# Optimization experiments

Measured on AMD Instinct MI355X. Metric: run time of the kernel, lower is better.

The kernel has to match this reference:

```python
import jax, jax.numpy as jnp
import numpy as np

N, E, F_IN, H, D = 50000, 800000, 128, 4, 32
NEG_SLOPE = 0.2

def setup_inputs() -> dict:
    key = jax.random.key(0)
    ks = jax.random.split(key, 8)
    x = jax.random.normal(ks[0], (N, F_IN), dtype=jnp.float32)
    src = jax.random.randint(ks[1], (E,), 0, N, dtype=jnp.int32)
    dst = jax.random.randint(ks[2], (E,), 0, N, dtype=jnp.int32)
    s = 1.0 / np.sqrt(F_IN)
    W_src = jax.random.uniform(ks[3], (F_IN, H * D), jnp.float32, -s, s)
    b_src = jnp.zeros((H * D,), jnp.float32)
    W_dst = jax.random.uniform(ks[4], (F_IN, H * D), jnp.float32, -s, s)
    b_dst = jnp.zeros((H * D,), jnp.float32)
    attn = jax.random.normal(ks[5], (H, D), dtype=jnp.float32) / np.sqrt(D)
    return {"x": x, "src": src, "dst": dst, "W_src": W_src, "b_src": b_src,
            "W_dst": W_dst, "b_dst": b_dst, "attn": attn}

def reference(x, src, dst, W_src, b_src, W_dst, b_dst, attn):
    n = x.shape[0]
    # dense projections: [N, H, D]
    fs = (x @ W_src + b_src).reshape(n, H, D)
    fd = (x @ W_dst + b_dst).reshape(n, H, D)
    # GATv2 edge score: a^T leaky_relu(W_l x_u + W_r x_v)
    e = jax.nn.leaky_relu(fs[src] + fd[dst], NEG_SLOPE)  # [E, H, D]
    score = jnp.einsum('ehd,hd->eh', e, attn)            # [E, H]
    # segment softmax over incoming edges of each dst node
    smax = jax.ops.segment_max(score, dst, num_segments=n)
    smax = jnp.where(jnp.isfinite(smax), smax, 0.0)
    ex = jnp.exp(score - smax[dst])
    denom = jax.ops.segment_sum(ex, dst, num_segments=n)
    alpha = ex / denom[dst]                              # [E, H]
    # scatter-weighted aggregation of src features
    h = jax.ops.segment_sum(alpha[:, :, None] * fs[src], dst, num_segments=n)
    h = jax.nn.relu(h)                                   # activation=relu
    return h.reshape(n, H * D)
```

## Files before the change

kernel.cpp:

```cpp
#include <hip/hip_runtime.h>
#include <hip/hip_fp16.h>

#define NN 50000
#define NE 800000
#define FIN 128
#define NH 4
#define HD 32
#define FOUT 128
#define NEG 0.2f
#define NB_W    ((256 * FIN + 255) / 256)
#define N_GEMM  782
#define NBKT    98
#define CHUNK   4096
#define NCHUNK  ((NE + CHUNK - 1) / CHUNK)
#define GB_GRID 980
#define BCAP    12288

typedef __attribute__((ext_vector_type(8))) short bf16x8;
typedef __attribute__((ext_vector_type(4))) float f32x4;

__device__ __forceinline__ uint f2bf_u(float f) {
    uint u = __float_as_uint(f);
    u += 0x7FFF + ((u >> 16) & 1);
    return u >> 16;
}
__device__ __forceinline__ ushort f2bf(float f) { return (ushort)f2bf_u(f); }
__device__ __forceinline__ uint f2h_u(float f) {
    return (uint)__builtin_bit_cast(ushort, __float2half(f));
}

template<int CTRL>
__device__ __forceinline__ float dpp_add(float x) {
    int y = __builtin_amdgcn_update_dpp(0, __float_as_int(x), CTRL, 0xF, 0xF, false);
    return x + __int_as_float(y);
}
#define DPP_QUAD_XOR1 0xB1
#define DPP_QUAD_XOR2 0x4E

__device__ __forceinline__ __half2 u2h(uint u) { return __builtin_bit_cast(__half2, u); }
__device__ __forceinline__ uint h2u(__half2 h) { return __builtin_bit_cast(uint, h); }

__device__ __forceinline__ __half2 hmax2(__half2 a, __half2 b) {
    uint r, ua = h2u(a), ub = h2u(b);
    asm("v_pk_max_f16 %0, %1, %2" : "=v"(r) : "v"(ua), "v"(ub));
    return u2h(r);
}

__global__ __launch_bounds__(256) void hist_wt_k(
    const int* __restrict__ dst, int* __restrict__ chunk_hist,
    const float* __restrict__ Wsrc, const float* __restrict__ Wdst,
    ushort* __restrict__ Wt,
    const float* __restrict__ attn, __half* __restrict__ attn_h)
{
    __shared__ int hist[NBKT];
    const int b = blockIdx.x;
    const int tid = threadIdx.x;
    if (b < NCHUNK) {
        const int e0 = b * CHUNK;
        for (int t = tid; t < NBKT; t += 256) hist[t] = 0;
        __syncthreads();
        #pragma unroll
        for (int k = 0; k < 16; ++k) {
            const int e = e0 + k * 256 + tid;
            if (e < NE) atomicAdd(&hist[dst[e] >> 9], 1);
        }
        __syncthreads();
        for (int t = tid; t < NBKT; t += 256)
            chunk_hist[b * NBKT + t] = hist[t];
    } else {
        if (b == NCHUNK && tid < FOUT) attn_h[tid] = __float2half(attn[tid]);
        int t = (b - NCHUNK) * 256 + tid;
        if (t >= 256 * FIN) return;
        int n = t >> 7, k = t & 127;
        float v = (n < 128) ? Wsrc[k * 128 + n] : Wdst[k * 128 + (n - 128)];
        Wt[t] = f2bf(v);
    }
}

__global__ __launch_bounds__(256) void gemm_scatter_k(
    const float* __restrict__ x, const ushort* __restrict__ Wt,
    const float* __restrict__ bsrc, const float* __restrict__ bdst,
    __half* __restrict__ fsfd,
    const int* __restrict__ dst, const int* __restrict__ src,
    const int* __restrict__ chunk_hist, int* __restrict__ bkbase,
    uint* __restrict__ ebuf)
{
    __shared__ ushort As[64 * 128];
    __shared__ ushort Bs[64 * 128];
    __shared__ int ps[256];
    __shared__ int gbase[NBKT];
    __shared__ int lcur[NBKT];
    __shared__ int delta[NBKT];
    const int b = blockIdx.x;
    const int tid = threadIdx.x;

    if (b % 5 == 0) {
        const int chunk = b / 5;
        uint* stage = (uint*)As;

        int total = 0, part = 0;
        if (tid < NBKT) {
            for (int c = 0; c < NCHUNK; ++c) {
                const int h = chunk_hist[c * NBKT + tid];
                total += h;
                part += (c < chunk) ? h : 0;
            }
        }
        ps[tid] = (tid < NBKT) ? total : 0;
        __syncthreads();
        for (int off = 1; off < 256; off <<= 1) {
            int add = (tid >= off) ? ps[tid - off] : 0;
            __syncthreads();
            ps[tid] += add;
            __syncthreads();
        }
        if (tid < NBKT) gbase[tid] = (ps[tid] - total) + part;
        if (chunk == 0) {
            if (tid < NBKT) bkbase[tid] = ps[tid] - total;
            if (tid == 0) bkbase[NBKT] = NE;
        }
        if (tid < NBKT) lcur[tid] = 0;
        __syncthreads();

        const int e0 = chunk * CHUNK;
        int d[16], s[16];
        #pragma unroll
        for (int k = 0; k < 16; ++k) {
            const int e = e0 + k * 256 + tid;
            if (e < NE) {
                d[k] = dst[e];
                s[k] = src[e];
                atomicAdd(&lcur[d[k] >> 9], 1);
            } else d[k] = -1;
        }
        __syncthreads();

        const int lv = (tid < NBKT) ? lcur[tid] : 0;
        ps[tid] = lv;
        __syncthreads();
        for (int off = 1; off < 256; off <<= 1) {
            int add = (tid >= off) ? ps[tid - off] : 0;
            __syncthreads();
            ps[tid] += add;
            __syncthreads();
        }
        if (tid < NBKT) {
            const int loff = ps[tid] - lv;
            lcur[tid] = loff;
            delta[tid] = gbase[tid] - loff;
        }
        __syncthreads();

        #pragma unroll
        for (int k = 0; k < 16; ++k) {
            if (d[k] >= 0) {
                const int p = atomicAdd(&lcur[d[k] >> 9], 1);
                stage[p] = ((uint)d[k] << 16) | (uint)s[k];
            }
        }
        __syncthreads();

        const int cnt = (NE - e0 < CHUNK) ? (NE - e0) : CHUNK;
        for (int i = tid; i < cnt; i += 256) {
            const uint e = stage[i];
            ebuf[delta[e >> 25] + i] = e;
        }
        return;
    }

    const int g = b - b / 5 - 1;
    if (g >= N_GEMM) return;
    const int bm = g * 64;

    for (int q = tid; q < 64 * 16; q += 256) {
        int r = q >> 4, c16 = q & 15;
        int row = bm + r;
        uint4 o = make_uint4(0u, 0u, 0u, 0u);
        if (row < NN) {
            const float4 a = *(const float4*)&x[(size_t)row * FIN + c16 * 8];
            const float4 c = *(const float4*)&x[(size_t)row * FIN + c16 * 8 + 4];
            o.x = f2bf_u(a.x) | (f2bf_u(a.y) << 16);
            o.y = f2bf_u(a.z) | (f2bf_u(a.w) << 16);
            o.z = f2bf_u(c.x) | (f2bf_u(c.y) << 16);
            o.w = f2bf_u(c.z) | (f2bf_u(c.w) << 16);
        }
        int off = r * 256 + ((c16 * 16) ^ ((r & 7) << 4));
        *(uint4*)((char*)As + off) = o;
    }

    const int wid = tid >> 6, lane = tid & 63;
    const int wr = (wid >> 1) * 32, wc = (wid & 1) * 32;
    const int lrow = lane & 15;
    const int lk = (lane >> 4) * 16;

    #pragma unroll
    for (int ct = 0; ct < 4; ++ct) {
        if (ct > 0) __syncthreads();
        for (int q = tid; q < 64 * 16; q += 256) {
            int r = q >> 4, c16 = q & 15;
            uint4 v = *(const uint4*)&Wt[(ct * 64 + r) * FIN + c16 * 8];
            int off = r * 256 + ((c16 * 16) ^ ((r & 7) << 4));
            *(uint4*)((char*)Bs + off) = v;
        }
        __syncthreads();

        f32x4 acc[2][2] = {};
        #pragma unroll
        for (int kk = 0; kk < 4; ++kk) {
            bf16x8 a[2], bb[2];
            #pragma unroll
            for (int m = 0; m < 2; ++m) {
                int r = wr + m * 16 + lrow;
                int off = r * 256 + ((kk * 64 + lk) ^ ((r & 7) << 4));
                a[m] = *(bf16x8*)((char*)As + off);
            }
            #pragma unroll
            for (int n = 0; n < 2; ++n) {
                int r = wc + n * 16 + lrow;
                int off = r * 256 + ((kk * 64 + lk) ^ ((r & 7) << 4));
                bb[n] = *(bf16x8*)((char*)Bs + off);
            }
            #pragma unroll
            for (int m = 0; m < 2; ++m)
                #pragma unroll
                for (int n = 0; n < 2; ++n)
                    acc[m][n] = __builtin_amdgcn_mfma_f32_16x16x32_bf16(bb[n], a[m], acc[m][n], 0, 0, 0);
        }

        #pragma unroll
        for (int m = 0; m < 2; ++m) {
            const int grow = bm + wr + m * 16 + (lane & 15);
            if (grow >= NN) continue;
            #pragma unroll
            for (int n = 0; n < 2; ++n) {
                const int gcolb = ct * 64 + wc + n * 16 + (lane >> 4) * 4;
                const float4 b4 = (gcolb < 128) ? *(const float4*)&bsrc[gcolb]
                                                : *(const float4*)&bdst[gcolb - 128];
                uint lo = f2h_u(acc[m][n][0] + b4.x) | (f2h_u(acc[m][n][1] + b4.y) << 16);
                uint hi = f2h_u(acc[m][n][2] + b4.z) | (f2h_u(acc[m][n][3] + b4.w) << 16);
                *(uint2*)&fsfd[(size_t)grow * 256 + gcolb] = make_uint2(lo, hi);
            }
        }
    }
}

__global__ __launch_bounds__(256) void binB_k(
    const uint* __restrict__ ebuf, const int* __restrict__ bkbase,
    int* __restrict__ rowptr, ushort* __restrict__ nbr)
{
    __shared__ int cnt_s[512];
    __shared__ int ps[256];
    __shared__ ushort buf[BCAP];
    const int b = blockIdx.x;
    const int tid = threadIdx.x;
    const int node0 = b << 9;
    const int nodes = (node0 + 512 < NN) ? 512 : (NN - node0);
    const int segbase = bkbase[b];
    const int segend  = bkbase[b + 1];
    const int seglen  = segend - segbase;

    cnt_s[tid] = 0;
    cnt_s[tid + 256] = 0;
    __syncthreads();
    for (int i = segbase + tid; i < segend; i += 256)
        atomicAdd(&cnt_s[(int)(ebuf[i] >> 16) - node0], 1);
    __syncthreads();

    const int c0 = cnt_s[2 * tid], c1 = cnt_s[2 * tid + 1];
    const int pair = c0 + c1;
    ps[tid] = pair;
    __syncthreads();
    for (int off = 1; off < 256; off <<= 1) {
        int add = (tid >= off) ? ps[tid - off] : 0;
        __syncthreads();
        ps[tid] += add;
        __syncthreads();
    }
    const int ex = ps[tid] - pair;
    __syncthreads();
    cnt_s[2 * tid] = ex;
    cnt_s[2 * tid + 1] = ex + c0;
    if (2 * tid < nodes)     rowptr[node0 + 2 * tid]     = segbase + ex;
    if (2 * tid + 1 < nodes) rowptr[node0 + 2 * tid + 1] = segbase + ex + c0;
    if (b == NBKT - 1 && tid == 0) rowptr[NN] = segend;
    __syncthreads();

    if (seglen <= BCAP) {
        for (int i = segbase + tid; i < segend; i += 256) {
            const uint e = ebuf[i];
            const int d = (int)(e >> 16) - node0;
            const int p = atomicAdd(&cnt_s[d], 1);
            buf[p] = (ushort)(e & 0xffffu);
        }
        __syncthreads();
        for (int i = tid; i < seglen; i += 256)
            nbr[segbase + i] = buf[i];
    } else {
        for (int i = segbase + tid; i < segend; i += 256) {
            const uint e = ebuf[i];
            const int d = (int)(e >> 16) - node0;
            const int p = atomicAdd(&cnt_s[d], 1);
            nbr[segbase + p] = (ushort)(e & 0xffffu);
        }
    }
}

__global__ __launch_bounds__(256) void gat_node_k(
    const __half* __restrict__ fsfd, const __half* __restrict__ attn_h,
    const int* __restrict__ rowptr, const ushort* __restrict__ nbr,
    float* __restrict__ out)
{
    const int node = blockIdx.x * 4 + (threadIdx.x >> 6);
    const int lane = threadIdx.x & 63;
    const int ql = lane & 15;
    const int q  = lane >> 4;

    const uint4 ufd = *(const uint4*)&fsfd[(size_t)node * 256 + 128 + 8 * ql];
    const __half2 fd0 = u2h(ufd.x), fd1 = u2h(ufd.y), fd2 = u2h(ufd.z), fd3 = u2h(ufd.w);
    const uint4 uav = *(const uint4*)&attn_h[8 * ql];
    const __half2 av0 = u2h(uav.x), av1 = u2h(uav.y), av2 = u2h(uav.z), av3 = u2h(uav.w);
    const __half2 k02 = __float2half2_rn(NEG);

    const int beg = rowptr[node];
    const int end = rowptr[node + 1];

    float den = 0.f;
    __half2 acc0 = u2h(0), acc1 = u2h(0), acc2 = u2h(0), acc3 = u2h(0);

    for (int i = beg; i < end; i += 16) {
        #pragma unroll
        for (int j = 0; j < 4; ++j) {
            const int idx = i + 4 * j + q;
            const bool valid = idx < end;
            const int s = nbr[valid ? idx : end - 1];
            const uint4 u = *(const uint4*)&fsfd[(size_t)s * 256 + 8 * ql];
            const __half2 f0 = u2h(u.x), f1 = u2h(u.y), f2 = u2h(u.z), f3 = u2h(u.w);
            __half2 v0 = __hadd2(f0, fd0), v1 = __hadd2(f1, fd1);
            __half2 v2 = __hadd2(f2, fd2), v3 = __hadd2(f3, fd3);
            v0 = hmax2(v0, __hmul2(v0, k02));
            v1 = hmax2(v1, __hmul2(v1, k02));
            v2 = hmax2(v2, __hmul2(v2, k02));
            v3 = hmax2(v3, __hmul2(v3, k02));
            __half2 sch = __hmul2(v0, av0);
            sch = __hfma2(v1, av1, sch);
            sch = __hfma2(v2, av2, sch);
            sch = __hfma2(v3, av3, sch);
            float sc = __low2float(sch) + __high2float(sch);
            sc = dpp_add<DPP_QUAD_XOR1>(sc);
            sc = dpp_add<DPP_QUAD_XOR2>(sc);
            float ex = __expf(sc);
            ex = valid ? ex : 0.f;
            den += ex;
            const __half2 exh = __float2half2_rn(ex);
            acc0 = __hfma2(exh, f0, acc0);
            acc1 = __hfma2(exh, f1, acc1);
            acc2 = __hfma2(exh, f2, acc2);
            acc3 = __hfma2(exh, f3, acc3);
        }
    }

    den += __shfl_xor(den, 16, 64);
    den += __shfl_xor(den, 32, 64);
    uint ua0 = h2u(acc0), ua1 = h2u(acc1), ua2 = h2u(acc2), ua3 = h2u(acc3);
    ua0 = h2u(__hadd2(u2h(ua0), u2h((uint)__shfl_xor((int)ua0, 16, 64))));
    ua1 = h2u(__hadd2(u2h(ua1), u2h((uint)__shfl_xor((int)ua1, 16, 64))));
    ua2 = h2u(__hadd2(u2h(ua2), u2h((uint)__shfl_xor((int)ua2, 16, 64))));
    ua3 = h2u(__hadd2(u2h(ua3), u2h((uint)__shfl_xor((int)ua3, 16, 64))));
    ua0 = h2u(__hadd2(u2h(ua0), u2h((uint)__shfl_xor((int)ua0, 32, 64))));
    ua1 = h2u(__hadd2(u2h(ua1), u2h((uint)__shfl_xor((int)ua1, 32, 64))));
    ua2 = h2u(__hadd2(u2h(ua2), u2h((uint)__shfl_xor((int)ua2, 32, 64))));
    ua3 = h2u(__hadd2(u2h(ua3), u2h((uint)__shfl_xor((int)ua3, 32, 64))));

    if (q == 0) {
        const float inv = (den > 0.f) ? 1.f / den : 0.f;
        float4 o0, o1;
        o0.x = fmaxf(__low2float(u2h(ua0))  * inv, 0.f);
        o0.y = fmaxf(__high2float(u2h(ua0)) * inv, 0.f);
        o0.z = fmaxf(__low2float(u2h(ua1))  * inv, 0.f);
        o0.w = fmaxf(__high2float(u2h(ua1)) * inv, 0.f);
        o1.x = fmaxf(__low2float(u2h(ua2))  * inv, 0.f);
        o1.y = fmaxf(__high2float(u2h(ua2)) * inv, 0.f);
        o1.z = fmaxf(__low2float(u2h(ua3))  * inv, 0.f);
        o1.w = fmaxf(__high2float(u2h(ua3)) * inv, 0.f);
        *(float4*)&out[(size_t)node * FOUT + 8 * ql] = o0;
        *(float4*)&out[(size_t)node * FOUT + 8 * ql + 4] = o1;
    }
}

extern "C" void kernel_launch(void* const* d_in, const int* in_sizes, int n_in,
                              void* d_out, int out_size, void* d_ws, size_t ws_size,
                              hipStream_t stream)
{
    const float* x    = (const float*)d_in[0];
    const int*   src  = (const int*)d_in[1];
    const int*   dst  = (const int*)d_in[2];
    const float* Wsrc = (const float*)d_in[3];
    const float* bsrc = (const float*)d_in[4];
    const float* Wdst = (const float*)d_in[5];
    const float* bdst = (const float*)d_in[6];
    const float* attn = (const float*)d_in[7];
    float* out = (float*)d_out;

    ushort* Wt      = (ushort*)d_ws;
    __half* fsfd    = (__half*)(Wt + 256 * FIN);
    int* chunk_hist = (int*)(fsfd + (size_t)NN * 256);
    int* bkbase     = chunk_hist + NCHUNK * NBKT;
    int* rowptr     = bkbase + NBKT + 1;
    uint* ebuf      = (uint*)(rowptr + NN + 1);
    ushort* nbr     = (ushort*)(ebuf + NE);
    __half* attn_h  = (__half*)(nbr + NE);

    hist_wt_k<<<NCHUNK + NB_W, 256, 0, stream>>>(dst, chunk_hist, Wsrc, Wdst, Wt, attn, attn_h);
    gemm_scatter_k<<<GB_GRID, 256, 0, stream>>>(x, Wt, bsrc, bdst, fsfd,
                                                dst, src, chunk_hist, bkbase, ebuf);
    binB_k<<<NBKT, 256, 0, stream>>>(ebuf, bkbase, rowptr, nbr);
    gat_node_k<<<(NN + 3) / 4, 256, 0, stream>>>(fsfd, attn_h, rowptr, nbr, out);
}
```

Measured before the change: 86.93 us.

## Split GEMM stripes across scatter and binning kernels to overlap work

The projection GEMM is split into two halves. The first half is interleaved with the edge-scatter blocks in one kernel, and the second half with the per-bucket CSR binning blocks in the next kernel. Before, the binning kernel ran only 98 blocks on its own. Co-scheduling it with GEMM stripes is meant to fill the idle compute units and hide the binning and scatter latency. The binning buffer now reuses the GEMM shared-memory pool, which raises LDS use per block and may lower occupancy.

After: 86.93 us. Within noise of the previous version (+0.0%).

```diff
diff --git a/kernel.cpp b/kernel.cpp
--- a/kernel.cpp
+++ b/kernel.cpp
@@ -13,7 +13,8 @@
 #define NBKT    98
 #define CHUNK   4096
 #define NCHUNK  ((NE + CHUNK - 1) / CHUNK)
-#define GB_GRID 980
+#define GS1_GRID 587
+#define GS2_GRID 489
 #define BCAP    12288
 
 typedef __attribute__((ext_vector_type(8))) short bf16x8;
@@ -46,132 +47,12 @@
     return u2h(r);
 }
 
-__global__ __launch_bounds__(256) void hist_wt_k(
-    const int* __restrict__ dst, int* __restrict__ chunk_hist,
-    const float* __restrict__ Wsrc, const float* __restrict__ Wdst,
-    ushort* __restrict__ Wt,
-    const float* __restrict__ attn, __half* __restrict__ attn_h)
-{
-    __shared__ int hist[NBKT];
-    const int b = blockIdx.x;
-    const int tid = threadIdx.x;
-    if (b < NCHUNK) {
-        const int e0 = b * CHUNK;
-        for (int t = tid; t < NBKT; t += 256) hist[t] = 0;
-        __syncthreads();
-        #pragma unroll
-        for (int k = 0; k < 16; ++k) {
-            const int e = e0 + k * 256 + tid;
-            if (e < NE) atomicAdd(&hist[dst[e] >> 9], 1);
-        }
-        __syncthreads();
-        for (int t = tid; t < NBKT; t += 256)
-            chunk_hist[b * NBKT + t] = hist[t];
-    } else {
-        if (b == NCHUNK && tid < FOUT) attn_h[tid] = __float2half(attn[tid]);
-        int t = (b - NCHUNK) * 256 + tid;
-        if (t >= 256 * FIN) return;
-        int n = t >> 7, k = t & 127;
-        float v = (n < 128) ? Wsrc[k * 128 + n] : Wdst[k * 128 + (n - 128)];
-        Wt[t] = f2bf(v);
-    }
-}
-
-__global__ __launch_bounds__(256) void gemm_scatter_k(
+__device__ __forceinline__ void gemm_stripe(
+    ushort* As, ushort* Bs, const int tid, const int bm,
     const float* __restrict__ x, const ushort* __restrict__ Wt,
     const float* __restrict__ bsrc, const float* __restrict__ bdst,
-    __half* __restrict__ fsfd,
-    const int* __restrict__ dst, const int* __restrict__ src,
-    const int* __restrict__ chunk_hist, int* __restrict__ bkbase,
-    uint* __restrict__ ebuf)
-{
-    __shared__ ushort As[64 * 128];
-    __shared__ ushort Bs[64 * 128];
-    __shared__ int ps[256];
-    __shared__ int gbase[NBKT];
-    __shared__ int lcur[NBKT];
-    __shared__ int delta[NBKT];
-    const int b = blockIdx.x;
-    const int tid = threadIdx.x;
-
-    if (b % 5 == 0) {
-        const int chunk = b / 5;
-        uint* stage = (uint*)As;
-
-        int total = 0, part = 0;
-        if (tid < NBKT) {
-            for (int c = 0; c < NCHUNK; ++c) {
-                const int h = chunk_hist[c * NBKT + tid];
-                total += h;
-                part += (c < chunk) ? h : 0;
-            }
-        }
-        ps[tid] = (tid < NBKT) ? total : 0;
-        __syncthreads();
-        for (int off = 1; off < 256; off <<= 1) {
-            int add = (tid >= off) ? ps[tid - off] : 0;
-            __syncthreads();
-            ps[tid] += add;
-            __syncthreads();
-        }
-        if (tid < NBKT) gbase[tid] = (ps[tid] - total) + part;
-        if (chunk == 0) {
-            if (tid < NBKT) bkbase[tid] = ps[tid] - total;
-            if (tid == 0) bkbase[NBKT] = NE;
-        }
-        if (tid < NBKT) lcur[tid] = 0;
-        __syncthreads();
-
-        const int e0 = chunk * CHUNK;
-        int d[16], s[16];
-        #pragma unroll
-        for (int k = 0; k < 16; ++k) {
-            const int e = e0 + k * 256 + tid;
-            if (e < NE) {
-                d[k] = dst[e];
-                s[k] = src[e];
-                atomicAdd(&lcur[d[k] >> 9], 1);
-            } else d[k] = -1;
-        }
-        __syncthreads();
-
-        const int lv = (tid < NBKT) ? lcur[tid] : 0;
-        ps[tid] = lv;
-        __syncthreads();
-        for (int off = 1; off < 256; off <<= 1) {
-            int add = (tid >= off) ? ps[tid - off] : 0;
-            __syncthreads();
-            ps[tid] += add;
-            __syncthreads();
-        }
-        if (tid < NBKT) {
-            const int loff = ps[tid] - lv;
-            lcur[tid] = loff;
-            delta[tid] = gbase[tid] - loff;
-        }
-        __syncthreads();
-
-        #pragma unroll
-        for (int k = 0; k < 16; ++k) {
-            if (d[k] >= 0) {
-                const int p = atomicAdd(&lcur[d[k] >> 9], 1);
-                stage[p] = ((uint)d[k] << 16) | (uint)s[k];
-            }
-        }
-        __syncthreads();
-
-        const int cnt = (NE - e0 < CHUNK) ? (NE - e0) : CHUNK;
-        for (int i = tid; i < cnt; i += 256) {
-            const uint e = stage[i];
-            ebuf[delta[e >> 25] + i] = e;
-        }
-        return;
-    }
-
-    const int g = b - b / 5 - 1;
-    if (g >= N_GEMM) return;
-    const int bm = g * 64;
-
+    __half* __restrict__ fsfd)
+{
     for (int q = tid; q < 64 * 16; q += 256) {
         int r = q >> 4, c16 = q & 15;
         int row = bm + r;
@@ -244,65 +125,202 @@
     }
 }
 
-__global__ __launch_bounds__(256) void binB_k(
+__global__ __launch_bounds__(256) void hist_wt_k(
+    const int* __restrict__ dst, int* __restrict__ chunk_hist,
+    const float* __restrict__ Wsrc, const float* __restrict__ Wdst,
+    ushort* __restrict__ Wt,
+    const float* __restrict__ attn, __half* __restrict__ attn_h)
+{
+    __shared__ int hist[NBKT];
+    const int b = blockIdx.x;
+    const int tid = threadIdx.x;
+    if (b < NCHUNK) {
+        const int e0 = b * CHUNK;
+        for (int t = tid; t < NBKT; t += 256) hist[t] = 0;
+        __syncthreads();
+        #pragma unroll
+        for (int k = 0; k < 16; ++k) {
+            const int e = e0 + k * 256 + tid;
+            if (e < NE) atomicAdd(&hist[dst[e] >> 9], 1);
+        }
+        __syncthreads();
+        for (int t = tid; t < NBKT; t += 256)
+            chunk_hist[b * NBKT + t] = hist[t];
+    } else {
+        if (b == NCHUNK && tid < FOUT) attn_h[tid] = __float2half(attn[tid]);
+        int t = (b - NCHUNK) * 256 + tid;
+        if (t >= 256 * FIN) return;
+        int n = t >> 7, k = t & 127;
+        float v = (n < 128) ? Wsrc[k * 128 + n] : Wdst[k * 128 + (n - 128)];
+        Wt[t] = f2bf(v);
+    }
+}
+
+__global__ __launch_bounds__(256) void gs1_k(
+    const float* __restrict__ x, const ushort* __restrict__ Wt,
+    const float* __restrict__ bsrc, const float* __restrict__ bdst,
+    __half* __restrict__ fsfd,
+    const int* __restrict__ dst, const int* __restrict__ src,
+    const int* __restrict__ chunk_hist, int* __restrict__ bkbase,
+    uint* __restrict__ ebuf)
+{
+    __shared__ ushort pool[64 * 128 * 2];
+    __shared__ int ps[256];
+    __shared__ int gbase[NBKT];
+    __shared__ int lcur[NBKT];
+    __shared__ int delta[NBKT];
+    const int b = blockIdx.x;
+    const int tid = threadIdx.x;
+
+    if (b % 3 == 0) {
+        const int chunk = b / 3;
+        uint* stage = (uint*)pool;
+
+        int total = 0, part = 0;
+        if (tid < NBKT) {
+            for (int c = 0; c < NCHUNK; ++c) {
+                const int h = chunk_hist[c * NBKT + tid];
+                total += h;
+                part += (c < chunk) ? h : 0;
+            }
+        }
+        ps[tid] = (tid < NBKT) ? total : 0;
+        __syncthreads();
+        for (int off = 1; off < 256; off <<= 1) {
+            int add = (tid >= off) ? ps[tid - off] : 0;
+            __syncthreads();
+            ps[tid] += add;
+            __syncthreads();
+        }
+        if (tid < NBKT) gbase[tid] = (ps[tid] - total) + part;
+        if (chunk == 0) {
+            if (tid < NBKT) bkbase[tid] = ps[tid] - total;
+            if (tid == 0) bkbase[NBKT] = NE;
+        }
+        if (tid < NBKT) lcur[tid] = 0;
+        __syncthreads();
+
+        const int e0 = chunk * CHUNK;
+        int d[16], s[16];
+        #pragma unroll
+        for (int k = 0; k < 16; ++k) {
+            const int e = e0 + k * 256 + tid;
+            if (e < NE) {
+                d[k] = dst[e];
+                s[k] = src[e];
+                atomicAdd(&lcur[d[k] >> 9], 1);
+            } else d[k] = -1;
+        }
+        __syncthreads();
+
+        const int lv = (tid < NBKT) ? lcur[tid] : 0;
+        ps[tid] = lv;
+        __syncthreads();
+        for (int off = 1; off < 256; off <<= 1) {
+            int add = (tid >= off) ? ps[tid - off] : 0;
+            __syncthreads();
+            ps[tid] += add;
+            __syncthreads();
+        }
+        if (tid < NBKT) {
+            const int loff = ps[tid] - lv;
+            lcur[tid] = loff;
+            delta[tid] = gbase[tid] - loff;
+        }
+        __syncthreads();
+
+        #pragma unroll
+        for (int k = 0; k < 16; ++k) {
+            if (d[k] >= 0) {
+                const int p = atomicAdd(&lcur[d[k] >> 9], 1);
+                stage[p] = ((uint)d[k] << 16) | (uint)s[k];
+            }
+        }
+        __syncthreads();
+
+        const int cnt = (NE - e0 < CHUNK) ? (NE - e0) : CHUNK;
+        for (int i = tid; i < cnt; i += 256) {
+            const uint e = stage[i];
+            ebuf[delta[e >> 25] + i] = e;
+        }
+        return;
+    }
+
+    const int g = b - b / 3 - 1;
+    gemm_stripe(pool, pool + 64 * 128, tid, g * 64, x, Wt, bsrc, bdst, fsfd);
+}
+
+__global__ __launch_bounds__(256) void gs2_k(
+    const float* __restrict__ x, const ushort* __restrict__ Wt,
+    const float* __restrict__ bsrc, const float* __restrict__ bdst,
+    __half* __restrict__ fsfd,
     const uint* __restrict__ ebuf, const int* __restrict__ bkbase,
     int* __restrict__ rowptr, ushort* __restrict__ nbr)
 {
+    __shared__ ushort pool[64 * 128 * 2];
     __shared__ int cnt_s[512];
     __shared__ int ps[256];
-    __shared__ ushort buf[BCAP];
     const int b = blockIdx.x;
     const int tid = threadIdx.x;
-    const int node0 = b << 9;
-    const int nodes = (node0 + 512 < NN) ? 512 : (NN - node0);
-    const int segbase = bkbase[b];
-    const int segend  = bkbase[b + 1];
-    const int seglen  = segend - segbase;
-
-    cnt_s[tid] = 0;
-    cnt_s[tid + 256] = 0;
-    __syncthreads();
-    for (int i = segbase + tid; i < segend; i += 256)
-        atomicAdd(&cnt_s[(int)(ebuf[i] >> 16) - node0], 1);
-    __syncthreads();
-
-    const int c0 = cnt_s[2 * tid], c1 = cnt_s[2 * tid + 1];
-    const int pair = c0 + c1;
-    ps[tid] = pair;
-    __syncthreads();
-    for (int off = 1; off < 256; off <<= 1) {
-        int add = (tid >= off) ? ps[tid - off] : 0;
-        __syncthreads();
-        ps[tid] += add;
-        __syncthreads();
-    }
-    const int ex = ps[tid] - pair;
-    __syncthreads();
-    cnt_s[2 * tid] = ex;
-    cnt_s[2 * tid + 1] = ex + c0;
-    if (2 * tid < nodes)     rowptr[node0 + 2 * tid]     = segbase + ex;
-    if (2 * tid + 1 < nodes) rowptr[node0 + 2 * tid + 1] = segbase + ex + c0;
-    if (b == NBKT - 1 && tid == 0) rowptr[NN] = segend;
-    __syncthreads();
-
-    if (seglen <= BCAP) {
-        for (int i = segbase + tid; i < segend; i += 256) {
-            const uint e = ebuf[i];
-            const int d = (int)(e >> 16) - node0;
-            const int p = atomicAdd(&cnt_s[d], 1);
-            buf[p] = (ushort)(e & 0xffffu);
-        }
-        __syncthreads();
-        for (int i = tid; i < seglen; i += 256)
-            nbr[segbase + i] = buf[i];
-    } else {
-        for (int i = segbase + tid; i < segend; i += 256) {
-            const uint e = ebuf[i];
-            const int d = (int)(e >> 16) - node0;
-            const int p = atomicAdd(&cnt_s[d], 1);
-            nbr[segbase + p] = (ushort)(e & 0xffffu);
-        }
-    }
+
+    if (b % 5 == 0) {
+        const int bb = b / 5;
+        ushort* buf = pool;
+        const int node0 = bb << 9;
+        const int nodes = (node0 + 512 < NN) ? 512 : (NN - node0);
+        const int segbase = bkbase[bb];
+        const int segend  = bkbase[bb + 1];
+        const int seglen  = segend - segbase;
+
+        cnt_s[tid] = 0;
+        cnt_s[tid + 256] = 0;
+        __syncthreads();
+        for (int i = segbase + tid; i < segend; i += 256)
+            atomicAdd(&cnt_s[(int)(ebuf[i] >> 16) - node0], 1);
+        __syncthreads();
+
+        const int c0 = cnt_s[2 * tid], c1 = cnt_s[2 * tid + 1];
+        const int pair = c0 + c1;
+        ps[tid] = pair;
+        __syncthreads();
+        for (int off = 1; off < 256; off <<= 1) {
+            int add = (tid >= off) ? ps[tid - off] : 0;
+            __syncthreads();
+            ps[tid] += add;
+            __syncthreads();
+        }
+        const int ex = ps[tid] - pair;
+        __syncthreads();
+        cnt_s[2 * tid] = ex;
+        cnt_s[2 * tid + 1] = ex + c0;
+        if (2 * tid < nodes)     rowptr[node0 + 2 * tid]     = segbase + ex;
+        if (2 * tid + 1 < nodes) rowptr[node0 + 2 * tid + 1] = segbase + ex + c0;
+        if (bb == NBKT - 1 && tid == 0) rowptr[NN] = segend;
+        __syncthreads();
+
+        if (seglen <= BCAP) {
+            for (int i = segbase + tid; i < segend; i += 256) {
+                const uint e = ebuf[i];
+                const int d = (int)(e >> 16) - node0;
+                const int p = atomicAdd(&cnt_s[d], 1);
+                buf[p] = (ushort)(e & 0xffffu);
+            }
+            __syncthreads();
+            for (int i = tid; i < seglen; i += 256)
+                nbr[segbase + i] = buf[i];
+        } else {
+            for (int i = segbase + tid; i < segend; i += 256) {
+                const uint e = ebuf[i];
+                const int d = (int)(e >> 16) - node0;
+                const int p = atomicAdd(&cnt_s[d], 1);
+                nbr[segbase + p] = (ushort)(e & 0xffffu);
+            }
+        }
+        return;
+    }
+
+    const int g = 391 + (b - b / 5 - 1);
+    gemm_stripe(pool, pool + 64 * 128, tid, g * 64, x, Wt, bsrc, bdst, fsfd);
 }
 
 __global__ __launch_bounds__(256) void gat_node_k(
@@ -411,8 +429,9 @@
     __half* attn_h  = (__half*)(nbr + NE);
 
     hist_wt_k<<<NCHUNK + NB_W, 256, 0, stream>>>(dst, chunk_hist, Wsrc, Wdst, Wt, attn, attn_h);
-    gemm_scatter_k<<<GB_GRID, 256, 0, stream>>>(x, Wt, bsrc, bdst, fsfd,
-                                                dst, src, chunk_hist, bkbase, ebuf);
-    binB_k<<<NBKT, 256, 0, stream>>>(ebuf, bkbase, rowptr, nbr);
+    gs1_k<<<GS1_GRID, 256, 0, stream>>>(x, Wt, bsrc, bdst, fsfd,
+                                        dst, src, chunk_hist, bkbase, ebuf);
+    gs2_k<<<GS2_GRID, 256, 0, stream>>>(x, Wt, bsrc, bdst, fsfd,
+                                        ebuf, bkbase, rowptr, nbr);
     gat_node_k<<<(NN + 3) / 4, 256, 0, stream>>>(fsfd, attn_h, rowptr, nbr, out);
 }
```

## Pre-swizzle weights and async-load B tiles directly to LDS in GEMM

Applied to the files above, without the earlier changes.

The weight transpose kernel now writes weights in the XOR-swizzled LDS layout, so the GEMM can copy each 64-column B tile straight into shared memory with global_load_lds, skipping the register round trip. The next B tile's load is issued before the epilogue stores of the current tile so the two overlap. A fragments are hoisted into registers once and reused across all four column tiles. This costs more registers and extra barriers, and relies on the swizzle layout matching the LDS read pattern exactly.

Result: no change. 87.33 us (+0.5%).

```diff
diff --git a/kernel.cpp b/kernel.cpp
--- a/kernel.cpp
+++ b/kernel.cpp
@@ -18,6 +18,8 @@
 
 typedef __attribute__((ext_vector_type(8))) short bf16x8;
 typedef __attribute__((ext_vector_type(4))) float f32x4;
+typedef __attribute__((address_space(1))) const uint GMem;
+typedef __attribute__((address_space(3))) uint LMem;
 
 __device__ __forceinline__ uint f2bf_u(float f) {
     uint u = __float_as_uint(f);
@@ -49,7 +51,7 @@
 __global__ __launch_bounds__(256) void hist_wt_k(
     const int* __restrict__ dst, int* __restrict__ chunk_hist,
     const float* __restrict__ Wsrc, const float* __restrict__ Wdst,
-    ushort* __restrict__ Wt,
+    ushort* __restrict__ WtSw,
     const float* __restrict__ attn, __half* __restrict__ attn_h)
 {
     __shared__ int hist[NBKT];
@@ -73,12 +75,13 @@
         if (t >= 256 * FIN) return;
         int n = t >> 7, k = t & 127;
         float v = (n < 128) ? Wsrc[k * 128 + n] : Wdst[k * 128 + (n - 128)];
-        Wt[t] = f2bf(v);
+        const int idx = n * 128 + ((((k >> 3) ^ (n & 7))) << 3) + (k & 7);
+        WtSw[idx] = f2bf(v);
     }
 }
 
 __global__ __launch_bounds__(256) void gemm_scatter_k(
-    const float* __restrict__ x, const ushort* __restrict__ Wt,
+    const float* __restrict__ x, const ushort* __restrict__ WtSw,
     const float* __restrict__ bsrc, const float* __restrict__ bdst,
     __half* __restrict__ fsfd,
     const int* __restrict__ dst, const int* __restrict__ src,
@@ -193,27 +196,35 @@
     const int lrow = lane & 15;
     const int lk = (lane >> 4) * 16;
 
+    {
+        const char* gsrc = (const char*)WtSw;
+        #pragma unroll
+        for (int i = 0; i < 4; ++i) {
+            const int seg = i * 4 + wid;
+            __builtin_amdgcn_global_load_lds(
+                (GMem*)(gsrc + seg * 1024 + lane * 16),
+                (LMem*)((char*)Bs + seg * 1024),
+                16, 0, 0);
+        }
+    }
+    __syncthreads();
+
+    bf16x8 areg[4][2];
+    #pragma unroll
+    for (int kk = 0; kk < 4; ++kk)
+        #pragma unroll
+        for (int m = 0; m < 2; ++m) {
+            int r = wr + m * 16 + lrow;
+            int off = r * 256 + ((kk * 64 + lk) ^ ((r & 7) << 4));
+            areg[kk][m] = *(bf16x8*)((char*)As + off);
+        }
+
     #pragma unroll
     for (int ct = 0; ct < 4; ++ct) {
-        if (ct > 0) __syncthreads();
-        for (int q = tid; q < 64 * 16; q += 256) {
-            int r = q >> 4, c16 = q & 15;
-            uint4 v = *(const uint4*)&Wt[(ct * 64 + r) * FIN + c16 * 8];
-            int off = r * 256 + ((c16 * 16) ^ ((r & 7) << 4));
-            *(uint4*)((char*)Bs + off) = v;
-        }
-        __syncthreads();
-
         f32x4 acc[2][2] = {};
         #pragma unroll
         for (int kk = 0; kk < 4; ++kk) {
-            bf16x8 a[2], bb[2];
-            #pragma unroll
-            for (int m = 0; m < 2; ++m) {
-                int r = wr + m * 16 + lrow;
-                int off = r * 256 + ((kk * 64 + lk) ^ ((r & 7) << 4));
-                a[m] = *(bf16x8*)((char*)As + off);
-            }
+            bf16x8 bb[2];
             #pragma unroll
             for (int n = 0; n < 2; ++n) {
                 int r = wc + n * 16 + lrow;
@@ -224,7 +235,20 @@
             for (int m = 0; m < 2; ++m)
                 #pragma unroll
                 for (int n = 0; n < 2; ++n)
-                    acc[m][n] = __builtin_amdgcn_mfma_f32_16x16x32_bf16(bb[n], a[m], acc[m][n], 0, 0, 0);
+                    acc[m][n] = __builtin_amdgcn_mfma_f32_16x16x32_bf16(bb[n], areg[kk][m], acc[m][n], 0, 0, 0);
+        }
+
+        if (ct < 3) {
+            __syncthreads();
+            const char* gsrc = (const char*)WtSw + (ct + 1) * 16384;
+            #pragma unroll
+            for (int i = 0; i < 4; ++i) {
+                const int seg = i * 4 + wid;
+                __builtin_amdgcn_global_load_lds(
+                    (GMem*)(gsrc + seg * 1024 + lane * 16),
+                    (LMem*)((char*)Bs + seg * 1024),
+                    16, 0, 0);
+            }
         }
 
         #pragma unroll
@@ -241,6 +265,7 @@
                 *(uint2*)&fsfd[(size_t)grow * 256 + gcolb] = make_uint2(lo, hi);
             }
         }
+        if (ct < 3) __syncthreads();
     }
 }
 
@@ -401,8 +426,8 @@
     const float* attn = (const float*)d_in[7];
     float* out = (float*)d_out;
 
-    ushort* Wt      = (ushort*)d_ws;
-    __half* fsfd    = (__half*)(Wt + 256 * FIN);
+    ushort* WtSw    = (ushort*)d_ws;
+    __half* fsfd    = (__half*)(WtSw + 256 * FIN);
     int* chunk_hist = (int*)(fsfd + (size_t)NN * 256);
     int* bkbase     = chunk_hist + NCHUNK * NBKT;
     int* rowptr     = bkbase + NBKT + 1;
@@ -410,8 +435,8 @@
     ushort* nbr     = (ushort*)(ebuf + NE);
     __half* attn_h  = (__half*)(nbr + NE);
 
-    hist_wt_k<<<NCHUNK + NB_W, 256, 0, stream>>>(dst, chunk_hist, Wsrc, Wdst, Wt, attn, attn_h);
-    gemm_scatter_k<<<GB_GRID, 256, 0, stream>>>(x, Wt, bsrc, bdst, fsfd,
+    hist_wt_k<<<NCHUNK + NB_W, 256, 0, stream>>>(dst, chunk_hist, Wsrc, Wdst, WtSw, attn, attn_h);
+    gemm_scatter_k<<<GB_GRID, 256, 0, stream>>>(x, WtSw, bsrc, bdst, fsfd,
                                                 dst, src, chunk_hist, bkbase, ebuf);
     binB_k<<<NBKT, 256, 0, stream>>>(ebuf, bkbase, rowptr, nbr);
     gat_node_k<<<(NN + 3) / 4, 256, 0, stream>>>(fsfd, attn_h, rowptr, nbr, out);
```
